# Kernel tuning notes

Measured on AMD Instinct MI355X. Metric: run time of the kernel, lower is better.

Reference implementation:

```python
import jax, jax.numpy as jnp
import numpy as np

MAX_SEQ_LEN = 512
PADDING_VALUE = -1.0
B, S_ENC, H, F = 128, 32, 768, 128


def setup_inputs() -> dict:
    key = jax.random.key(0)
    ks = jax.random.split(key, 9)
    s = 1.0 / np.sqrt(H)  # torch-style uniform-ish scale, use scaled normal
    return {
        "H_o": jax.random.normal(ks[0], (B, S_ENC, H), jnp.float32),
        "H_n": jax.random.normal(ks[1], (1, B, H), jnp.float32),
        "T": jax.random.randint(ks[2], (B,), 0, MAX_SEQ_LEN, jnp.int64),
        "W_ih": jax.random.normal(ks[3], (3 * H, H), jnp.float32) * s,
        "W_hh": jax.random.normal(ks[4], (3 * H, H), jnp.float32) * s,
        "b_ih": jax.random.normal(ks[5], (3 * H,), jnp.float32) * s,
        "b_hh": jax.random.normal(ks[6], (3 * H,), jnp.float32) * s,
        "W_lin": jax.random.normal(ks[7], (F, H), jnp.float32) * s,
        "b_lin": jax.random.normal(ks[8], (F,), jnp.float32) * s,
    }


def _gru_cell(x, h, W_ih, W_hh, b_ih, b_hh):
    # torch GRU gate ordering: reset, update, new
    gi = x @ W_ih.T + b_ih  # (B, 3H)
    gh = h @ W_hh.T + b_hh
    gi_r, gi_z, gi_n = jnp.split(gi, 3, axis=-1)
    gh_r, gh_z, gh_n = jnp.split(gh, 3, axis=-1)
    r = jax.nn.sigmoid(gi_r + gh_r)
    z = jax.nn.sigmoid(gi_z + gh_z)
    n = jnp.tanh(gi_n + r * gh_n)
    return (1.0 - z) * n + z * h


def reference(H_o, H_n, T, W_ih, W_hh, b_ih, b_hh, W_lin, b_lin):
    x0 = H_o[:, -1, :]  # (B, H): last encoder output seeds the decoder
    h0 = H_n[0]         # (B, H): single-layer hidden state

    def step(carry, _):
        x, h = carry
        h_new = _gru_cell(x, h, W_ih, W_hh, b_ih, b_hh)
        # output of single-layer GRU == new hidden; fed back as next input
        return (h_new, h_new), h_new

    _, Y = jax.lax.scan(step, (x0, h0), None, length=MAX_SEQ_LEN)  # (S, B, H)
    X_hat = jnp.einsum("sbh,fh->sbf", Y, W_lin) + b_lin            # (S, B, F)
    X_hat = jnp.transpose(X_hat, (1, 0, 2))[:, ::-1, :]            # (B, S, F), time-reversed
    valid = jnp.arange(MAX_SEQ_LEN)[None, :] < T[:, None]          # (B, S)
    return jnp.where(valid[:, :, None], X_hat, PADDING_VALUE)
```

## Files before the change

kernel.cpp:

```cpp
#include <hip/hip_runtime.h>

typedef _Float16 f16;
typedef _Float16 half8 __attribute__((ext_vector_type(8)));
typedef float f32x4 __attribute__((ext_vector_type(4)));
typedef int i32x4 __attribute__((ext_vector_type(4)));

#define SEQ 512
#define NB 128
#define NH 768
#define NFEAT 128
#define NGRP 4
#define BG 32
#define NCOL 48
#define NWG (NGRP*NCOL)
#define KW 192
#define NKT 6
#define NRES 27

#define OFF_WIH   0LL
#define OFF_WHH   3538944LL
#define OFF_WLIN  7077888LL
#define OFF_XBUF  7274496LL
#define OFF_HBUF  7471104LL
#define OFF_CTR   7667712LL
#define OFF_Y     7684096LL
#define OFF_TN    108347392LL
#define WS_NEED   (OFF_TN + 1024)

__global__ void fill_sentinel(float* out, long long n) {
  long long i = (long long)blockIdx.x * blockDim.x + threadIdx.x;
  long long stride = (long long)gridDim.x * blockDim.x;
  for (; i < n; i += stride) out[i] = -2.0f;
}

__global__ void prep_kernel(const float* __restrict__ Ho, const float* __restrict__ Hn,
                            const unsigned int* __restrict__ Traw,
                            const float* __restrict__ Wih, const float* __restrict__ Whh,
                            const float* __restrict__ Wlin,
                            f16* __restrict__ wih16, f16* __restrict__ whh16,
                            f16* __restrict__ wlin16,
                            f16* __restrict__ xbuf, f16* __restrict__ hbuf,
                            int* __restrict__ Tn)
{
  long long idx = (long long)blockIdx.x * blockDim.x + threadIdx.x;
  long long stride = (long long)gridDim.x * blockDim.x;
  for (long long i = idx; i < 2304LL * 768LL; i += stride) {
    wih16[i] = (f16)Wih[i];
    whh16[i] = (f16)Whh[i];
  }
  for (long long i = idx; i < 128LL * 768LL; i += stride) {
    long long b = i / 768, h = i % 768;
    wlin16[i] = (f16)Wlin[i];
    xbuf[i] = (f16)Ho[(b * 32 + 31) * 768 + h];
    hbuf[i] = (f16)Hn[i];
  }
  if (blockIdx.x == 0 && threadIdx.x < 128) {
    bool allz = true;
    for (int i = 0; i < 64; ++i) allz = allz && (Traw[2 * i + 1] == 0u);
    int t = threadIdx.x;
    Tn[t] = allz ? (int)Traw[2 * t] : (int)Traw[t];
  }
}

__global__ void __launch_bounds__(256, 1)
gru_kernel(const f16* __restrict__ wih16, const f16* __restrict__ whh16,
           const f16* __restrict__ xbuf, const f16* __restrict__ hbuf,
           const float* __restrict__ Hn,
           const float* __restrict__ b_ih, const float* __restrict__ b_hh,
           f16* __restrict__ Y, unsigned int* __restrict__ ctr)
{
  const int wg  = blockIdx.x;
  const int g   = wg & (NGRP - 1);
  const int c   = wg >> 2;
  const int tid = threadIdx.x;
  const int lane = tid & 63;
  const int wv  = tid >> 6;
  const int j0  = c * 16;
  const int ks  = wv * KW;
  const int bbase = g * BG;

  __shared__ __align__(16) f16 wbuf[4 * NRES * 512];
  __shared__ f32x4 pb[4 * 12 * 64];

  const int n15 = lane & 15;
  const int kg8 = (lane >> 4) * 8;

#pragma unroll
  for (int gt = 0; gt < 6; ++gt) {
    const f16* Wsrc = (gt < 3) ? wih16 : whh16;
    const f16* base = Wsrc + (size_t)((gt % 3) * 768 + j0 + n15) * NH + ks + kg8;
#pragma unroll
    for (int kt = 0; kt < NKT; ++kt) {
      int idx = gt * 6 + kt;
      if (idx < NRES)
        *(i32x4*)(wbuf + (wv * NRES + idx) * 512 + lane * 8) =
            *(const i32x4*)(base + kt * 32);
    }
  }

  const int gb = tid >> 4;
  const int gj = tid & 15;
  const int jglob = j0 + gj;
  float hc0 = Hn[(size_t)(bbase + gb) * NH + jglob];
  float hc1 = Hn[(size_t)(bbase + 16 + gb) * NH + jglob];
  const float bi_r = b_ih[jglob], bi_z = b_ih[768 + jglob], bi_n = b_ih[1536 + jglob];
  const float bh_r = b_hh[jglob], bh_z = b_hh[768 + jglob], bh_n = b_hh[1536 + jglob];

  const size_t arow0 = (size_t)(bbase + n15) * NH + ks + kg8;
  const size_t arow1 = arow0 + (size_t)16 * NH;
  const size_t ywr0  = (size_t)(bbase + gb) * NH + jglob;
  const size_t ywr1  = ywr0 + (size_t)16 * NH;

  const int l4r = (((gb >> 2) * 16 + gj) << 2) + (gb & 3);

  const f16* b4 = whh16 + (size_t)(1 * 768 + j0 + n15) * NH + ks + kg8;
  const f16* b5 = whh16 + (size_t)(2 * 768 + j0 + n15) * NH + ks + kg8;

  unsigned int* cbase = ctr + ((size_t)g << 9);

  __syncthreads();

  for (int s = 0; s < SEQ; ++s) {
    const f16* hsrc = (s == 0) ? hbuf : (Y + (size_t)(s - 1) * (NB * NH));
    const f16* xsrc = (s == 0) ? xbuf : hsrc;

    half8 A0[NKT], A1[NKT];
#pragma unroll
    for (int kt = 0; kt < NKT; ++kt) {
      A0[kt] = *(const half8*)(xsrc + arow0 + kt * 32);
      A1[kt] = *(const half8*)(xsrc + arow1 + kt * 32);
    }
    half8 I43 = *(const half8*)(b4 + 3 * 32);
    half8 I44 = *(const half8*)(b4 + 4 * 32);
    half8 I45 = *(const half8*)(b4 + 5 * 32);
    half8 I50 = *(const half8*)(b5 + 0 * 32);
    half8 I51 = *(const half8*)(b5 + 1 * 32);
    half8 I52 = *(const half8*)(b5 + 2 * 32);
    half8 I53 = *(const half8*)(b5 + 3 * 32);
    half8 I54 = *(const half8*)(b5 + 4 * 32);
    half8 I55 = *(const half8*)(b5 + 5 * 32);

    f32x4 acc0[6], acc1[6];
#pragma unroll
    for (int gt = 0; gt < 6; ++gt) {
      acc0[gt] = (f32x4){0.f, 0.f, 0.f, 0.f};
      acc1[gt] = (f32x4){0.f, 0.f, 0.f, 0.f};
    }

    const f16* wb = wbuf + (size_t)(wv * NRES) * 512 + lane * 8;

#pragma unroll
    for (int gt = 0; gt < 3; ++gt) {
#pragma unroll
      for (int kt = 0; kt < NKT; ++kt) {
        half8 B = *(const half8*)(wb + (gt * 6 + kt) * 512);
        acc0[gt] = __builtin_amdgcn_mfma_f32_16x16x32_f16(A0[kt], B, acc0[gt], 0, 0, 0);
        acc1[gt] = __builtin_amdgcn_mfma_f32_16x16x32_f16(A1[kt], B, acc1[gt], 0, 0, 0);
      }
    }

    if (s == 0) {
#pragma unroll
      for (int kt = 0; kt < NKT; ++kt) {
        A0[kt] = *(const half8*)(hbuf + arow0 + kt * 32);
        A1[kt] = *(const half8*)(hbuf + arow1 + kt * 32);
      }
    }

#pragma unroll
    for (int kt = 0; kt < NKT; ++kt) {
      half8 B = *(const half8*)(wb + (18 + kt) * 512);
      acc0[3] = __builtin_amdgcn_mfma_f32_16x16x32_f16(A0[kt], B, acc0[3], 0, 0, 0);
      acc1[3] = __builtin_amdgcn_mfma_f32_16x16x32_f16(A1[kt], B, acc1[3], 0, 0, 0);
    }
#pragma unroll
    for (int kt = 0; kt < 3; ++kt) {
      half8 B = *(const half8*)(wb + (24 + kt) * 512);
      acc0[4] = __builtin_amdgcn_mfma_f32_16x16x32_f16(A0[kt], B, acc0[4], 0, 0, 0);
      acc1[4] = __builtin_amdgcn_mfma_f32_16x16x32_f16(A1[kt], B, acc1[4], 0, 0, 0);
    }
    acc0[4] = __builtin_amdgcn_mfma_f32_16x16x32_f16(A0[3], I43, acc0[4], 0, 0, 0);
    acc1[4] = __builtin_amdgcn_mfma_f32_16x16x32_f16(A1[3], I43, acc1[4], 0, 0, 0);
    acc0[4] = __builtin_amdgcn_mfma_f32_16x16x32_f16(A0[4], I44, acc0[4], 0, 0, 0);
    acc1[4] = __builtin_amdgcn_mfma_f32_16x16x32_f16(A1[4], I44, acc1[4], 0, 0, 0);
    acc0[4] = __builtin_amdgcn_mfma_f32_16x16x32_f16(A0[5], I45, acc0[4], 0, 0, 0);
    acc1[4] = __builtin_amdgcn_mfma_f32_16x16x32_f16(A1[5], I45, acc1[4], 0, 0, 0);
    acc0[5] = __builtin_amdgcn_mfma_f32_16x16x32_f16(A0[0], I50, acc0[5], 0, 0, 0);
    acc1[5] = __builtin_amdgcn_mfma_f32_16x16x32_f16(A1[0], I50, acc1[5], 0, 0, 0);
    acc0[5] = __builtin_amdgcn_mfma_f32_16x16x32_f16(A0[1], I51, acc0[5], 0, 0, 0);
    acc1[5] = __builtin_amdgcn_mfma_f32_16x16x32_f16(A1[1], I51, acc1[5], 0, 0, 0);
    acc0[5] = __builtin_amdgcn_mfma_f32_16x16x32_f16(A0[2], I52, acc0[5], 0, 0, 0);
    acc1[5] = __builtin_amdgcn_mfma_f32_16x16x32_f16(A1[2], I52, acc1[5], 0, 0, 0);
    acc0[5] = __builtin_amdgcn_mfma_f32_16x16x32_f16(A0[3], I53, acc0[5], 0, 0, 0);
    acc1[5] = __builtin_amdgcn_mfma_f32_16x16x32_f16(A1[3], I53, acc1[5], 0, 0, 0);
    acc0[5] = __builtin_amdgcn_mfma_f32_16x16x32_f16(A0[4], I54, acc0[5], 0, 0, 0);
    acc1[5] = __builtin_amdgcn_mfma_f32_16x16x32_f16(A1[4], I54, acc1[5], 0, 0, 0);
    acc0[5] = __builtin_amdgcn_mfma_f32_16x16x32_f16(A0[5], I55, acc0[5], 0, 0, 0);
    acc1[5] = __builtin_amdgcn_mfma_f32_16x16x32_f16(A1[5], I55, acc1[5], 0, 0, 0);

#pragma unroll
    for (int gt = 0; gt < 6; ++gt) {
      pb[wv * 768 + gt * 64 + lane]        = acc0[gt];
      pb[wv * 768 + (6 + gt) * 64 + lane]  = acc1[gt];
    }
    __syncthreads();

    const float* pf = (const float*)pb;
#pragma unroll
    for (int p = 0; p < 2; ++p) {
      float gir = bi_r, giz = bi_z, gin = bi_n, ghr = bh_r, ghz = bh_z, ghn = bh_n;
#pragma unroll
      for (int ww = 0; ww < 4; ++ww) {
        const float* q = pf + ww * 3072 + p * 1536 + l4r;
        gir += q[0];    giz += q[256];  gin += q[512];
        ghr += q[768];  ghz += q[1024]; ghn += q[1280];
      }
      float hcarry = p ? hc1 : hc0;
      float rr = 1.f / (1.f + __expf(-(gir + ghr)));
      float zz = 1.f / (1.f + __expf(-(giz + ghz)));
      float xn = gin + rr * ghn;
      float nn = 1.f - 2.f / (__expf(2.f * xn) + 1.f);
      float hnew = (1.f - zz) * nn + zz * hcarry;
      if (p) hc1 = hnew; else hc0 = hnew;

      unsigned int u = (unsigned int)__builtin_bit_cast(unsigned short, (f16)hnew);
      unsigned int partner = (unsigned int)__shfl_xor((int)u, 1);
      if ((tid & 1) == 0) {
        unsigned int val = u | (partner << 16);
        size_t off = p ? ywr1 : ywr0;
        unsigned int* dst = (unsigned int*)(Y + (size_t)s * (NB * NH) + off);
        __hip_atomic_store(dst, val, __ATOMIC_RELAXED, __HIP_MEMORY_SCOPE_AGENT);
      }
    }

    __syncthreads();
    if (tid == 0) {
      unsigned int* cp = cbase + s;
      __hip_atomic_fetch_add(cp, 1u, __ATOMIC_RELAXED, __HIP_MEMORY_SCOPE_AGENT);
      while (__hip_atomic_load(cp, __ATOMIC_RELAXED, __HIP_MEMORY_SCOPE_AGENT) < NCOL)
        __builtin_amdgcn_s_sleep(1);
    }
    __syncthreads();
  }
}

__global__ void __launch_bounds__(256)
proj_kernel(const f16* __restrict__ Y, const f16* __restrict__ wlin16,
            const float* __restrict__ b_lin, const int* __restrict__ Tn,
            float* __restrict__ out)
{
  const int tid = threadIdx.x;
  const int lane = tid & 63;
  const int wv = tid >> 6;
  const int r0 = blockIdx.x * 64 + wv * 16;
  const int n15 = lane & 15;
  const int kg8 = (lane >> 4) * 8;
  const size_t arow_off = (size_t)(r0 + n15) * NH + kg8;

  f32x4 acc[8];
#pragma unroll
  for (int nf = 0; nf < 8; ++nf) acc[nf] = (f32x4){0.f, 0.f, 0.f, 0.f};

  for (int kt = 0; kt < 24; ++kt) {
    half8 a = *(const half8*)(Y + arow_off + kt * 32);
#pragma unroll
    for (int nf = 0; nf < 8; ++nf) {
      half8 bfr = *(const half8*)(wlin16 + (size_t)(nf * 16 + n15) * NH + kt * 32 + kg8);
      acc[nf] = __builtin_amdgcn_mfma_f32_16x16x32_f16(a, bfr, acc[nf], 0, 0, 0);
    }
  }

#pragma unroll
  for (int nf = 0; nf < 8; ++nf) {
    int fcol = nf * 16 + n15;
    float bl = b_lin[fcol];
#pragma unroll
    for (int r = 0; r < 4; ++r) {
      int row = r0 + (lane >> 4) * 4 + r;
      int s = row >> 7, b = row & 127;
      int t = 511 - s;
      float v = (t < Tn[b]) ? (acc[nf][r] + bl) : -1.0f;
      out[((size_t)b * 512 + t) * NFEAT + fcol] = v;
    }
  }
}

extern "C" void kernel_launch(void* const* d_in, const int* in_sizes, int n_in,
                              void* d_out, int out_size, void* d_ws, size_t ws_size,
                              hipStream_t stream) {
  const float* Ho   = (const float*)d_in[0];
  const float* Hn   = (const float*)d_in[1];
  const unsigned int* Traw = (const unsigned int*)d_in[2];
  const float* Wih  = (const float*)d_in[3];
  const float* Whh  = (const float*)d_in[4];
  const float* bih  = (const float*)d_in[5];
  const float* bhh  = (const float*)d_in[6];
  const float* Wlin = (const float*)d_in[7];
  const float* blin = (const float*)d_in[8];
  float* out = (float*)d_out;

  if (ws_size < (size_t)WS_NEED) {
    fill_sentinel<<<1024, 256, 0, stream>>>(out, (long long)out_size);
    return;
  }

  char* ws = (char*)d_ws;
  f16* wih16  = (f16*)(ws + OFF_WIH);
  f16* whh16  = (f16*)(ws + OFF_WHH);
  f16* wlin16 = (f16*)(ws + OFF_WLIN);
  f16* xbuf   = (f16*)(ws + OFF_XBUF);
  f16* hbuf   = (f16*)(ws + OFF_HBUF);
  unsigned int* ctr = (unsigned int*)(ws + OFF_CTR);
  f16* Y      = (f16*)(ws + OFF_Y);
  int* Tn     = (int*)(ws + OFF_TN);

  hipMemsetAsync(ctr, 0, NGRP * SEQ * sizeof(unsigned int), stream);
  prep_kernel<<<512, 256, 0, stream>>>(Ho, Hn, Traw, Wih, Whh, Wlin,
                                       wih16, whh16, wlin16, xbuf, hbuf, Tn);
  gru_kernel<<<NWG, 256, 0, stream>>>(wih16, whh16, xbuf, hbuf, Hn, bih, bhh, Y, ctr);
  proj_kernel<<<1024, 256, 0, stream>>>(Y, wlin16, blin, Tn, out);
}
```

Measured before the change: 2.111 ms.

## Halve GRU workgroups with 8-wave blocks and read weights directly from global

Reorganizes the recurrent GRU kernel so each workgroup uses 512 threads covering two 16-column tiles, halving the number of workgroups that must synchronize each timestep. It drops the LDS weight cache and register-held weight tiles, loading all weight fragments from global memory every step instead. This aims to cut inter-workgroup sync cost and simplify the inner loop. The risk is repeated weight traffic through the cache hierarchy on every timestep.

```diff
diff --git a/kernel.cpp b/kernel.cpp
--- a/kernel.cpp
+++ b/kernel.cpp
@@ -11,11 +11,10 @@
 #define NFEAT 128
 #define NGRP 4
 #define BG 32
-#define NCOL 48
+#define NCOL 24
 #define NWG (NGRP*NCOL)
 #define KW 192
 #define NKT 6
-#define NRES 27
 
 #define OFF_WIH   0LL
 #define OFF_WHH   3538944LL
@@ -62,7 +61,7 @@
   }
 }
 
-__global__ void __launch_bounds__(256, 1)
+__global__ void __launch_bounds__(512, 1)
 gru_kernel(const f16* __restrict__ wih16, const f16* __restrict__ whh16,
            const f16* __restrict__ xbuf, const f16* __restrict__ hbuf,
            const float* __restrict__ Hn,
@@ -75,32 +74,29 @@
   const int tid = threadIdx.x;
   const int lane = tid & 63;
   const int wv  = tid >> 6;
-  const int j0  = c * 16;
-  const int ks  = wv * KW;
+  const int ct  = wv >> 2;
+  const int kw  = wv & 3;
+  const int j0  = c * 32 + ct * 16;
+  const int ks  = kw * KW;
   const int bbase = g * BG;
 
-  __shared__ __align__(16) f16 wbuf[4 * NRES * 512];
-  __shared__ f32x4 pb[4 * 12 * 64];
+  __shared__ f32x4 pb[8 * 12 * 64];
 
   const int n15 = lane & 15;
   const int kg8 = (lane >> 4) * 8;
 
-#pragma unroll
-  for (int gt = 0; gt < 6; ++gt) {
-    const f16* Wsrc = (gt < 3) ? wih16 : whh16;
-    const f16* base = Wsrc + (size_t)((gt % 3) * 768 + j0 + n15) * NH + ks + kg8;
-#pragma unroll
-    for (int kt = 0; kt < NKT; ++kt) {
-      int idx = gt * 6 + kt;
-      if (idx < NRES)
-        *(i32x4*)(wbuf + (wv * NRES + idx) * 512 + lane * 8) =
-            *(const i32x4*)(base + kt * 32);
-    }
-  }
-
-  const int gb = tid >> 4;
-  const int gj = tid & 15;
-  const int jglob = j0 + gj;
+  const f16* wb0 = wih16 + (size_t)(0 * 768 + j0 + n15) * NH + ks + kg8;
+  const f16* wb1 = wih16 + (size_t)(1 * 768 + j0 + n15) * NH + ks + kg8;
+  const f16* wb2 = wih16 + (size_t)(2 * 768 + j0 + n15) * NH + ks + kg8;
+  const f16* wb3 = whh16 + (size_t)(0 * 768 + j0 + n15) * NH + ks + kg8;
+  const f16* wb4 = whh16 + (size_t)(1 * 768 + j0 + n15) * NH + ks + kg8;
+  const f16* wb5 = whh16 + (size_t)(2 * 768 + j0 + n15) * NH + ks + kg8;
+
+  const int ctg = tid >> 8;
+  const int r8  = tid & 255;
+  const int gb  = r8 >> 4;
+  const int gj  = r8 & 15;
+  const int jglob = c * 32 + ctg * 16 + gj;
   float hc0 = Hn[(size_t)(bbase + gb) * NH + jglob];
   float hc1 = Hn[(size_t)(bbase + 16 + gb) * NH + jglob];
   const float bi_r = b_ih[jglob], bi_z = b_ih[768 + jglob], bi_n = b_ih[1536 + jglob];
@@ -113,12 +109,7 @@
 
   const int l4r = (((gb >> 2) * 16 + gj) << 2) + (gb & 3);
 
-  const f16* b4 = whh16 + (size_t)(1 * 768 + j0 + n15) * NH + ks + kg8;
-  const f16* b5 = whh16 + (size_t)(2 * 768 + j0 + n15) * NH + ks + kg8;
-
   unsigned int* cbase = ctr + ((size_t)g << 9);
-
-  __syncthreads();
 
   for (int s = 0; s < SEQ; ++s) {
     const f16* hsrc = (s == 0) ? hbuf : (Y + (size_t)(s - 1) * (NB * NH));
@@ -130,15 +121,6 @@
       A0[kt] = *(const half8*)(xsrc + arow0 + kt * 32);
       A1[kt] = *(const half8*)(xsrc + arow1 + kt * 32);
     }
-    half8 I43 = *(const half8*)(b4 + 3 * 32);
-    half8 I44 = *(const half8*)(b4 + 4 * 32);
-    half8 I45 = *(const half8*)(b4 + 5 * 32);
-    half8 I50 = *(const half8*)(b5 + 0 * 32);
-    half8 I51 = *(const half8*)(b5 + 1 * 32);
-    half8 I52 = *(const half8*)(b5 + 2 * 32);
-    half8 I53 = *(const half8*)(b5 + 3 * 32);
-    half8 I54 = *(const half8*)(b5 + 4 * 32);
-    half8 I55 = *(const half8*)(b5 + 5 * 32);
 
     f32x4 acc0[6], acc1[6];
 #pragma unroll
@@ -147,16 +129,17 @@
       acc1[gt] = (f32x4){0.f, 0.f, 0.f, 0.f};
     }
 
-    const f16* wb = wbuf + (size_t)(wv * NRES) * 512 + lane * 8;
-
-#pragma unroll
-    for (int gt = 0; gt < 3; ++gt) {
-#pragma unroll
-      for (int kt = 0; kt < NKT; ++kt) {
-        half8 B = *(const half8*)(wb + (gt * 6 + kt) * 512);
-        acc0[gt] = __builtin_amdgcn_mfma_f32_16x16x32_f16(A0[kt], B, acc0[gt], 0, 0, 0);
-        acc1[gt] = __builtin_amdgcn_mfma_f32_16x16x32_f16(A1[kt], B, acc1[gt], 0, 0, 0);
-      }
+#pragma unroll
+    for (int kt = 0; kt < NKT; ++kt) {
+      half8 B0 = *(const half8*)(wb0 + kt * 32);
+      half8 B1 = *(const half8*)(wb1 + kt * 32);
+      half8 B2 = *(const half8*)(wb2 + kt * 32);
+      acc0[0] = __builtin_amdgcn_mfma_f32_16x16x32_f16(A0[kt], B0, acc0[0], 0, 0, 0);
+      acc1[0] = __builtin_amdgcn_mfma_f32_16x16x32_f16(A1[kt], B0, acc1[0], 0, 0, 0);
+      acc0[1] = __builtin_amdgcn_mfma_f32_16x16x32_f16(A0[kt], B1, acc0[1], 0, 0, 0);
+      acc1[1] = __builtin_amdgcn_mfma_f32_16x16x32_f16(A1[kt], B1, acc1[1], 0, 0, 0);
+      acc0[2] = __builtin_amdgcn_mfma_f32_16x16x32_f16(A0[kt], B2, acc0[2], 0, 0, 0);
+      acc1[2] = __builtin_amdgcn_mfma_f32_16x16x32_f16(A1[kt], B2, acc1[2], 0, 0, 0);
     }
 
     if (s == 0) {
@@ -169,39 +152,21 @@
 
 #pragma unroll
     for (int kt = 0; kt < NKT; ++kt) {
-      half8 B = *(const half8*)(wb + (18 + kt) * 512);
-      acc0[3] = __builtin_amdgcn_mfma_f32_16x16x32_f16(A0[kt], B, acc0[3], 0, 0, 0);
-      acc1[3] = __builtin_amdgcn_mfma_f32_16x16x32_f16(A1[kt], B, acc1[3], 0, 0, 0);
-    }
-#pragma unroll
-    for (int kt = 0; kt < 3; ++kt) {
-      half8 B = *(const half8*)(wb + (24 + kt) * 512);
-      acc0[4] = __builtin_amdgcn_mfma_f32_16x16x32_f16(A0[kt], B, acc0[4], 0, 0, 0);
-      acc1[4] = __builtin_amdgcn_mfma_f32_16x16x32_f16(A1[kt], B, acc1[4], 0, 0, 0);
-    }
-    acc0[4] = __builtin_amdgcn_mfma_f32_16x16x32_f16(A0[3], I43, acc0[4], 0, 0, 0);
-    acc1[4] = __builtin_amdgcn_mfma_f32_16x16x32_f16(A1[3], I43, acc1[4], 0, 0, 0);
-    acc0[4] = __builtin_amdgcn_mfma_f32_16x16x32_f16(A0[4], I44, acc0[4], 0, 0, 0);
-    acc1[4] = __builtin_amdgcn_mfma_f32_16x16x32_f16(A1[4], I44, acc1[4], 0, 0, 0);
-    acc0[4] = __builtin_amdgcn_mfma_f32_16x16x32_f16(A0[5], I45, acc0[4], 0, 0, 0);
-    acc1[4] = __builtin_amdgcn_mfma_f32_16x16x32_f16(A1[5], I45, acc1[4], 0, 0, 0);
-    acc0[5] = __builtin_amdgcn_mfma_f32_16x16x32_f16(A0[0], I50, acc0[5], 0, 0, 0);
-    acc1[5] = __builtin_amdgcn_mfma_f32_16x16x32_f16(A1[0], I50, acc1[5], 0, 0, 0);
-    acc0[5] = __builtin_amdgcn_mfma_f32_16x16x32_f16(A0[1], I51, acc0[5], 0, 0, 0);
-    acc1[5] = __builtin_amdgcn_mfma_f32_16x16x32_f16(A1[1], I51, acc1[5], 0, 0, 0);
-    acc0[5] = __builtin_amdgcn_mfma_f32_16x16x32_f16(A0[2], I52, acc0[5], 0, 0, 0);
-    acc1[5] = __builtin_amdgcn_mfma_f32_16x16x32_f16(A1[2], I52, acc1[5], 0, 0, 0);
-    acc0[5] = __builtin_amdgcn_mfma_f32_16x16x32_f16(A0[3], I53, acc0[5], 0, 0, 0);
-    acc1[5] = __builtin_amdgcn_mfma_f32_16x16x32_f16(A1[3], I53, acc1[5], 0, 0, 0);
-    acc0[5] = __builtin_amdgcn_mfma_f32_16x16x32_f16(A0[4], I54, acc0[5], 0, 0, 0);
-    acc1[5] = __builtin_amdgcn_mfma_f32_16x16x32_f16(A1[4], I54, acc1[5], 0, 0, 0);
-    acc0[5] = __builtin_amdgcn_mfma_f32_16x16x32_f16(A0[5], I55, acc0[5], 0, 0, 0);
-    acc1[5] = __builtin_amdgcn_mfma_f32_16x16x32_f16(A1[5], I55, acc1[5], 0, 0, 0);
+      half8 B3 = *(const half8*)(wb3 + kt * 32);
+      half8 B4 = *(const half8*)(wb4 + kt * 32);
+      half8 B5 = *(const half8*)(wb5 + kt * 32);
+      acc0[3] = __builtin_amdgcn_mfma_f32_16x16x32_f16(A0[kt], B3, acc0[3], 0, 0, 0);
+      acc1[3] = __builtin_amdgcn_mfma_f32_16x16x32_f16(A1[kt], B3, acc1[3], 0, 0, 0);
+      acc0[4] = __builtin_amdgcn_mfma_f32_16x16x32_f16(A0[kt], B4, acc0[4], 0, 0, 0);
+      acc1[4] = __builtin_amdgcn_mfma_f32_16x16x32_f16(A1[kt], B4, acc1[4], 0, 0, 0);
+      acc0[5] = __builtin_amdgcn_mfma_f32_16x16x32_f16(A0[kt], B5, acc0[5], 0, 0, 0);
+      acc1[5] = __builtin_amdgcn_mfma_f32_16x16x32_f16(A1[kt], B5, acc1[5], 0, 0, 0);
+    }
 
 #pragma unroll
     for (int gt = 0; gt < 6; ++gt) {
-      pb[wv * 768 + gt * 64 + lane]        = acc0[gt];
-      pb[wv * 768 + (6 + gt) * 64 + lane]  = acc1[gt];
+      pb[(wv * 12 + gt) * 64 + lane]     = acc0[gt];
+      pb[(wv * 12 + 6 + gt) * 64 + lane] = acc1[gt];
     }
     __syncthreads();
 
@@ -210,8 +175,8 @@
     for (int p = 0; p < 2; ++p) {
       float gir = bi_r, giz = bi_z, gin = bi_n, ghr = bh_r, ghz = bh_z, ghn = bh_n;
 #pragma unroll
-      for (int ww = 0; ww < 4; ++ww) {
-        const float* q = pf + ww * 3072 + p * 1536 + l4r;
+      for (int k4 = 0; k4 < 4; ++k4) {
+        const float* q = pf + (((ctg * 4 + k4) * 12 + p * 6) << 8) + l4r;
         gir += q[0];    giz += q[256];  gin += q[512];
         ghr += q[768];  ghz += q[1024]; ghn += q[1280];
       }
@@ -317,6 +282,6 @@
   hipMemsetAsync(ctr, 0, NGRP * SEQ * sizeof(unsigned int), stream);
   prep_kernel<<<512, 256, 0, stream>>>(Ho, Hn, Traw, Wih, Whh, Wlin,
                                        wih16, whh16, wlin16, xbuf, hbuf, Tn);
-  gru_kernel<<<NWG, 256, 0, stream>>>(wih16, whh16, xbuf, hbuf, Hn, bih, bhh, Y, ctr);
+  gru_kernel<<<NWG, 512, 0, stream>>>(wih16, whh16, xbuf, hbuf, Hn, bih, bhh, Y, ctr);
   proj_kernel<<<1024, 256, 0, stream>>>(Y, wlin16, blin, Tn, out);
 }
```

After: 2.853 ms. 35.1% more time.
